# Optimization experiments

Hardware: AMD Instinct MI355X
Metric: run time of the kernel (lower is better)

## Reference

```python
import jax, jax.numpy as jnp
import numpy as np

HIDDEN = 1024
HEADS = 16
HEAD = HIDDEN // HEADS


def _ternary_weight(key, shape):
    g = jax.random.normal(key, shape, dtype=jnp.float32)
    return jnp.where(jnp.abs(g) < 0.6, 0.0, jnp.sign(g)).astype(jnp.float32)


def setup_inputs() -> dict:
    key = jax.random.key(0)
    ks = jax.random.split(key, 10)
    x = jax.random.normal(ks[0], (2, 2048, HIDDEN), dtype=jnp.float32)
    d = {"x": x}
    names = ["q", "k", "v", "o"]
    for i, n in enumerate(names):
        d[f"w_{n}"] = _ternary_weight(ks[1 + i], (HIDDEN, HIDDEN))
        d[f"s_{n}"] = jnp.float32(0.02)  # per-layer dequant scale
        d[f"b_{n}"] = jax.random.normal(ks[5 + i], (HIDDEN,), dtype=jnp.float32) * 0.02
    return d


def _tlin(x, w, s, b):
    # dequantized ternary linear: x @ (s * w).T + b
    return jnp.einsum("bsh,oh->bso", x, w) * s + b


def reference(x, w_q, s_q, b_q, w_k, s_k, b_k, w_v, s_v, b_v, w_o, s_o, b_o):
    B, S, H = x.shape
    def split_heads(t):
        return t.reshape(B, S, HEADS, HEAD).transpose(0, 2, 1, 3)  # [B, nH, S, hd]
    q = split_heads(_tlin(x, w_q, s_q, b_q))
    k = split_heads(_tlin(x, w_k, s_k, b_k))
    v = split_heads(_tlin(x, w_v, s_v, b_v))
    scores = jnp.einsum("bhqd,bhkd->bhqk", q, k) / jnp.sqrt(jnp.float32(HEAD))
    attn = jax.nn.softmax(scores, axis=-1)
    ctx = jnp.einsum("bhqk,bhkd->bhqd", attn, v)
    ctx = ctx.transpose(0, 2, 1, 3).reshape(B, S, H)
    return _tlin(ctx, w_o, s_o, b_o)
```

## Files before the change

kernel.cpp:

```cpp
#include <hip/hip_runtime.h>
#include <hip/hip_bf16.h>

typedef unsigned short u16;
typedef __bf16 bf16x8 __attribute__((ext_vector_type(8)));
typedef float f32x4 __attribute__((ext_vector_type(4)));
typedef unsigned short u16x8 __attribute__((ext_vector_type(8)));
typedef unsigned short u16x4 __attribute__((ext_vector_type(4)));

__device__ inline u16 f2bf(float f) {
    union { float f; unsigned u; } v; v.f = f;
    unsigned r = v.u + 0x7fffu + ((v.u >> 16) & 1u);
    return (u16)(r >> 16);
}

__device__ inline float bf2f(u16 b) {
    union { unsigned u; float f; } v; v.u = ((unsigned)b) << 16;
    return v.f;
}

__global__ void convert_kernel(const float* __restrict__ x,
                               const float* __restrict__ wq, const float* __restrict__ wk,
                               const float* __restrict__ wv, const float* __restrict__ wo,
                               u16* __restrict__ dst) {
    long g = (long)blockIdx.x * blockDim.x + threadIdx.x;
    const float* src; long base;
    const long GX = 1048576, GW = 262144;
    if (g < GX)            { src = x;  base = 0; }
    else if (g < GX + GW)  { src = wq; base = GX; }
    else if (g < GX + 2*GW){ src = wk; base = GX + GW; }
    else if (g < GX + 3*GW){ src = wv; base = GX + 2*GW; }
    else                   { src = wo; base = GX + 3*GW; }
    long rel = g - base;
    float4 v = reinterpret_cast<const float4*>(src)[rel];
    ushort4 o;
    o.x = f2bf(v.x); o.y = f2bf(v.y); o.z = f2bf(v.z); o.w = f2bf(v.w);
    reinterpret_cast<ushort4*>(dst)[g] = o;
}

#define LDP 72

__device__ inline void gemm_mainloop(const u16* __restrict__ A, const u16* __restrict__ W,
                                     int t0, int n0, u16* As, u16* Bs, f32x4 acc[4][4]) {
    const int tid = threadIdx.x;
    const int wid = tid >> 6, lane = tid & 63, quad = lane >> 4, ln = lane & 15;
    const int wm = wid >> 1, wn = wid & 1;
#pragma unroll
    for (int im = 0; im < 4; im++)
#pragma unroll
        for (int in = 0; in < 4; in++) acc[im][in] = (f32x4){0.f, 0.f, 0.f, 0.f};

    for (int k0 = 0; k0 < 1024; k0 += 64) {
#pragma unroll
        for (int i = 0; i < 4; i++) {
            int c = i * 256 + tid;
            int row = c >> 3, kc = c & 7;
            u16x8 av = *reinterpret_cast<const u16x8*>(A + (long)(t0 + row) * 1024 + k0 + kc * 8);
            u16x8 bv = *reinterpret_cast<const u16x8*>(W + (long)(n0 + row) * 1024 + k0 + kc * 8);
            *reinterpret_cast<u16x8*>(As + row * LDP + kc * 8) = av;
            *reinterpret_cast<u16x8*>(Bs + row * LDP + kc * 8) = bv;
        }
        __syncthreads();
#pragma unroll
        for (int ks = 0; ks < 2; ks++) {
            bf16x8 af[4], bf[4];
#pragma unroll
            for (int im = 0; im < 4; im++)
                af[im] = *reinterpret_cast<const bf16x8*>(As + (wm * 64 + im * 16 + ln) * LDP + ks * 32 + quad * 8);
#pragma unroll
            for (int in = 0; in < 4; in++)
                bf[in] = *reinterpret_cast<const bf16x8*>(Bs + (wn * 64 + in * 16 + ln) * LDP + ks * 32 + quad * 8);
#pragma unroll
            for (int im = 0; im < 4; im++)
#pragma unroll
                for (int in = 0; in < 4; in++)
                    acc[im][in] = __builtin_amdgcn_mfma_f32_16x16x32_bf16(af[im], bf[in], acc[im][in], 0, 0, 0);
        }
        __syncthreads();
    }
}

__global__ void qkv_gemm(const u16* __restrict__ x_bf,
                         const u16* __restrict__ wq, const u16* __restrict__ wk, const u16* __restrict__ wv,
                         const float* __restrict__ sq, const float* __restrict__ sk, const float* __restrict__ sv,
                         const float* __restrict__ bq, const float* __restrict__ bk, const float* __restrict__ bv,
                         u16* __restrict__ q_ws, u16* __restrict__ k_ws, u16* __restrict__ v_ws) {
    __shared__ u16 As[128 * LDP];
    __shared__ u16 Bs[128 * LDP];
    const int z = blockIdx.z;
    const u16* W   = (z == 0) ? wq : (z == 1) ? wk : wv;
    const float* sp = (z == 0) ? sq : (z == 1) ? sk : sv;
    const float* bp = (z == 0) ? bq : (z == 1) ? bk : bv;
    u16* dst = (z == 0) ? q_ws : (z == 1) ? k_ws : v_ws;
    const float extra = (z == 0) ? 0.125f : 1.0f;
    const int t0 = blockIdx.x * 128, n0 = blockIdx.y * 128;

    f32x4 acc[4][4];
    gemm_mainloop(x_bf, W, t0, n0, As, Bs, acc);

    const int tid = threadIdx.x;
    const int wid = tid >> 6, lane = tid & 63, quad = lane >> 4, ln = lane & 15;
    const int wm = wid >> 1, wn = wid & 1;
    const float s = sp[0] * extra;
#pragma unroll
    for (int in = 0; in < 4; in++) {
        int col = n0 + wn * 64 + in * 16 + ln;
        float bias = bp[col] * extra;
        int h = col >> 6, d = col & 63;
#pragma unroll
        for (int im = 0; im < 4; im++) {
            int rbase = t0 + wm * 64 + im * 16 + quad * 4;
#pragma unroll
            for (int j = 0; j < 4; j++) {
                int t = rbase + j;
                int b = t >> 11, ss = t & 2047;
                int bh = b * 16 + h;
                float val = acc[im][in][j] * s + bias;
                long idx = (z < 2) ? ((long)(bh * 2048 + ss) * 64 + d)
                                   : ((long)(bh * 64 + d) * 2048 + ss);
                dst[idx] = f2bf(val);
            }
        }
    }
}

__global__ void attn_kernel(const u16* __restrict__ q_ws, const u16* __restrict__ k_ws,
                            const u16* __restrict__ v_ws, u16* __restrict__ ctx) {
    __shared__ u16 Kt[64 * LDP];
    __shared__ u16 Vt[64 * LDP];
    __shared__ u16 Pt[128 * LDP];

    const int tid = threadIdx.x;
    const int wid = tid >> 6, lane = tid & 63, quad = lane >> 4, ln = lane & 15;
    const int bh = blockIdx.y;
    const int q0 = blockIdx.x * 128;
    const u16* qbase = q_ws + (long)bh * 2048 * 64;
    const u16* kbase = k_ws + (long)bh * 2048 * 64;
    const u16* vbase = v_ws + (long)bh * 64 * 2048;

    bf16x8 aq[2][2];
#pragma unroll
    for (int qt = 0; qt < 2; qt++)
#pragma unroll
        for (int ks = 0; ks < 2; ks++)
            aq[qt][ks] = *reinterpret_cast<const bf16x8*>(
                qbase + (long)(q0 + wid * 32 + qt * 16 + ln) * 64 + ks * 32 + quad * 8);

    f32x4 acc_o[2][4];
    float lsum[2] = {0.f, 0.f};
#pragma unroll
    for (int qt = 0; qt < 2; qt++)
#pragma unroll
        for (int dt = 0; dt < 4; dt++) acc_o[qt][dt] = (f32x4){0.f, 0.f, 0.f, 0.f};

    u16x8 kreg[2], vreg[2];
#pragma unroll
    for (int i = 0; i < 2; i++) {
        int c = i * 256 + tid;
        int row = c >> 3, kc = c & 7;
        kreg[i] = *reinterpret_cast<const u16x8*>(kbase + (long)row * 64 + kc * 8);
        vreg[i] = *reinterpret_cast<const u16x8*>(vbase + (long)row * 2048 + kc * 8);
    }

    for (int kt = 0; kt < 2048; kt += 64) {
#pragma unroll
        for (int i = 0; i < 2; i++) {
            int c = i * 256 + tid;
            int row = c >> 3, kc = c & 7;
            *reinterpret_cast<u16x8*>(Kt + row * LDP + kc * 8) = kreg[i];
            *reinterpret_cast<u16x8*>(Vt + row * LDP + kc * 8) = vreg[i];
        }
        if (kt + 64 < 2048) {
#pragma unroll
            for (int i = 0; i < 2; i++) {
                int c = i * 256 + tid;
                int row = c >> 3, kc = c & 7;
                kreg[i] = *reinterpret_cast<const u16x8*>(kbase + (long)(kt + 64 + row) * 64 + kc * 8);
                vreg[i] = *reinterpret_cast<const u16x8*>(vbase + (long)row * 2048 + (kt + 64) + kc * 8);
            }
        }
        __syncthreads();

#pragma unroll
        for (int k8 = 0; k8 < 4; k8++) {
            bf16x8 a0 = *reinterpret_cast<const bf16x8*>(Kt + (k8 * 16 + ln) * LDP + quad * 8);
            bf16x8 a1 = *reinterpret_cast<const bf16x8*>(Kt + (k8 * 16 + ln) * LDP + 32 + quad * 8);
#pragma unroll
            for (int qt = 0; qt < 2; qt++) {
                f32x4 t = (f32x4){0.f, 0.f, 0.f, 0.f};
                t = __builtin_amdgcn_mfma_f32_16x16x32_bf16(a0, aq[qt][0], t, 0, 0, 0);
                t = __builtin_amdgcn_mfma_f32_16x16x32_bf16(a1, aq[qt][1], t, 0, 0, 0);
                float p0 = __expf(t[0]), p1 = __expf(t[1]), p2 = __expf(t[2]), p3 = __expf(t[3]);
                u16x4 w;
                w.x = f2bf(p0); w.y = f2bf(p1); w.z = f2bf(p2); w.w = f2bf(p3);
                lsum[qt] += bf2f(w.x) + bf2f(w.y) + bf2f(w.z) + bf2f(w.w);
                *reinterpret_cast<u16x4*>(
                    Pt + (wid * 32 + qt * 16 + ln) * LDP + k8 * 16 + quad * 4) = w;
            }
        }

#pragma unroll
        for (int step = 0; step < 2; step++) {
            bf16x8 ap[2];
#pragma unroll
            for (int qt = 0; qt < 2; qt++)
                ap[qt] = *reinterpret_cast<const bf16x8*>(
                    Pt + (wid * 32 + qt * 16 + ln) * LDP + step * 32 + quad * 8);
#pragma unroll
            for (int dt = 0; dt < 4; dt++) {
                bf16x8 bv = *reinterpret_cast<const bf16x8*>(
                    Vt + (dt * 16 + ln) * LDP + step * 32 + quad * 8);
#pragma unroll
                for (int qt = 0; qt < 2; qt++)
                    acc_o[qt][dt] = __builtin_amdgcn_mfma_f32_16x16x32_bf16(ap[qt], bv, acc_o[qt][dt], 0, 0, 0);
            }
        }
        __syncthreads();
    }

    const int b = bh >> 4, h = bh & 15;
#pragma unroll
    for (int qt = 0; qt < 2; qt++) {
        float lt = lsum[qt];
        lt += __shfl_xor(lt, 16, 64);
        lt += __shfl_xor(lt, 32, 64);
#pragma unroll
        for (int j = 0; j < 4; j++) {
            float rinv = 1.0f / __shfl(lt, quad * 4 + j, 64);
            int t = b * 2048 + q0 + wid * 32 + qt * 16 + quad * 4 + j;
#pragma unroll
            for (int dt = 0; dt < 4; dt++) {
                float val = acc_o[qt][dt][j] * rinv;
                ctx[(long)t * 1024 + h * 64 + dt * 16 + ln] = f2bf(val);
            }
        }
    }
}

__global__ void o_gemm(const u16* __restrict__ ctx, const u16* __restrict__ wo,
                       const float* __restrict__ so, const float* __restrict__ bo,
                       float* __restrict__ out) {
    __shared__ u16 As[128 * LDP];
    __shared__ u16 Bs[128 * LDP];
    const int t0 = blockIdx.x * 128, n0 = blockIdx.y * 128;
    f32x4 acc[4][4];
    gemm_mainloop(ctx, wo, t0, n0, As, Bs, acc);

    const int tid = threadIdx.x;
    const int wid = tid >> 6, lane = tid & 63, quad = lane >> 4, ln = lane & 15;
    const int wm = wid >> 1, wn = wid & 1;
    const float s = so[0];
#pragma unroll
    for (int in = 0; in < 4; in++) {
        int col = n0 + wn * 64 + in * 16 + ln;
        float bias = bo[col];
#pragma unroll
        for (int im = 0; im < 4; im++) {
            int rbase = t0 + wm * 64 + im * 16 + quad * 4;
#pragma unroll
            for (int j = 0; j < 4; j++)
                out[(long)(rbase + j) * 1024 + col] = acc[im][in][j] * s + bias;
        }
    }
}

extern "C" void kernel_launch(void* const* d_in, const int* in_sizes, int n_in,
                              void* d_out, int out_size, void* d_ws, size_t ws_size,
                              hipStream_t stream) {
    const float* x   = (const float*)d_in[0];
    const float* w_q = (const float*)d_in[1];
    const float* s_q = (const float*)d_in[2];
    const float* b_q = (const float*)d_in[3];
    const float* w_k = (const float*)d_in[4];
    const float* s_k = (const float*)d_in[5];
    const float* b_k = (const float*)d_in[6];
    const float* w_v = (const float*)d_in[7];
    const float* s_v = (const float*)d_in[8];
    const float* b_v = (const float*)d_in[9];
    const float* w_o = (const float*)d_in[10];
    const float* s_o = (const float*)d_in[11];
    const float* b_o = (const float*)d_in[12];

    if (ws_size < (size_t)50331648) return;

    u16* ws     = (u16*)d_ws;
    u16* x_bf   = ws;
    u16* wq_bf  = x_bf  + 4194304;
    u16* wk_bf  = wq_bf + 1048576;
    u16* wv_bf  = wk_bf + 1048576;
    u16* wo_bf  = wv_bf + 1048576;
    u16* q_ws   = wo_bf + 1048576;
    u16* k_ws   = q_ws  + 4194304;
    u16* v_ws   = k_ws  + 4194304;
    u16* ctx_ws = v_ws  + 4194304;

    convert_kernel<<<dim3(8192), dim3(256), 0, stream>>>(x, w_q, w_k, w_v, w_o, ws);
    qkv_gemm<<<dim3(32, 8, 3), dim3(256), 0, stream>>>(x_bf, wq_bf, wk_bf, wv_bf,
                                                       s_q, s_k, s_v, b_q, b_k, b_v,
                                                       q_ws, k_ws, v_ws);
    attn_kernel<<<dim3(16, 32), dim3(256), 0, stream>>>(q_ws, k_ws, v_ws, ctx_ws);
    o_gemm<<<dim3(32, 8), dim3(256), 0, stream>>>(ctx_ws, wo_bf, s_o, b_o, (float*)d_out);
}
```

Measured before the change: 222.6 us.

## Use direct global-to-LDS loads with XOR swizzle, exp2 softmax, 512-thread attention

The GEMM mainloop now stages A and W tiles with global_load_lds straight into an unpadded, XOR-swizzled LDS layout instead of going through registers, and the fragment reads use the same swizzle to avoid bank conflicts. The Q scale folds in log2(e) so attention can use the hardware exp2 instruction in place of __expf. The attention kernel switches to 512 threads, with each wave handling 16 query rows instead of 32, which halves per-wave registers but doubles the waves sharing each K/V tile. These are several independent changes that trade code simplicity for less staging overhead and more parallelism.

Result: faster. 207.7 us (-6.7%).

```diff
diff --git a/kernel.cpp b/kernel.cpp
--- a/kernel.cpp
+++ b/kernel.cpp
@@ -3,19 +3,14 @@
 
 typedef unsigned short u16;
 typedef __bf16 bf16x8 __attribute__((ext_vector_type(8)));
+typedef __bf16 bf16x4 __attribute__((ext_vector_type(4)));
 typedef float f32x4 __attribute__((ext_vector_type(4)));
 typedef unsigned short u16x8 __attribute__((ext_vector_type(8)));
-typedef unsigned short u16x4 __attribute__((ext_vector_type(4)));
 
 __device__ inline u16 f2bf(float f) {
     union { float f; unsigned u; } v; v.f = f;
     unsigned r = v.u + 0x7fffu + ((v.u >> 16) & 1u);
     return (u16)(r >> 16);
-}
-
-__device__ inline float bf2f(u16 b) {
-    union { unsigned u; float f; } v; v.u = ((unsigned)b) << 16;
-    return v.f;
 }
 
 __global__ void convert_kernel(const float* __restrict__ x,
@@ -37,8 +32,6 @@
     reinterpret_cast<ushort4*>(dst)[g] = o;
 }
 
-#define LDP 72
-
 __device__ inline void gemm_mainloop(const u16* __restrict__ A, const u16* __restrict__ W,
                                      int t0, int n0, u16* As, u16* Bs, f32x4 acc[4][4]) {
     const int tid = threadIdx.x;
@@ -52,28 +45,40 @@
     for (int k0 = 0; k0 < 1024; k0 += 64) {
 #pragma unroll
         for (int i = 0; i < 4; i++) {
-            int c = i * 256 + tid;
-            int row = c >> 3, kc = c & 7;
-            u16x8 av = *reinterpret_cast<const u16x8*>(A + (long)(t0 + row) * 1024 + k0 + kc * 8);
-            u16x8 bv = *reinterpret_cast<const u16x8*>(W + (long)(n0 + row) * 1024 + k0 + kc * 8);
-            *reinterpret_cast<u16x8*>(As + row * LDP + kc * 8) = av;
-            *reinterpret_cast<u16x8*>(Bs + row * LDP + kc * 8) = bv;
+            int chunk = wid * 4 + i;
+            int b = chunk * 1024 + lane * 16;
+            int row = b >> 7;
+            int cb = (b & 127) ^ ((row & 7) << 4);
+            const u16* gA = A + (long)(t0 + row) * 1024 + k0 + (cb >> 1);
+            const u16* gB = W + (long)(n0 + row) * 1024 + k0 + (cb >> 1);
+            __builtin_amdgcn_global_load_lds((const __attribute__((address_space(1))) void*)gA,
+                                             (__attribute__((address_space(3))) void*)(As + chunk * 512),
+                                             16, 0, 0);
+            __builtin_amdgcn_global_load_lds((const __attribute__((address_space(1))) void*)gB,
+                                             (__attribute__((address_space(3))) void*)(Bs + chunk * 512),
+                                             16, 0, 0);
         }
         __syncthreads();
 #pragma unroll
         for (int ks = 0; ks < 2; ks++) {
-            bf16x8 af[4], bf[4];
+            bf16x8 af[4], bfr[4];
+#pragma unroll
+            for (int im = 0; im < 4; im++) {
+                int r = wm * 64 + im * 16 + ln;
+                int byt = (r * 128 + ks * 64 + quad * 16) ^ ((r & 7) << 4);
+                af[im] = *reinterpret_cast<const bf16x8*>((const char*)As + byt);
+            }
+#pragma unroll
+            for (int in = 0; in < 4; in++) {
+                int r = wn * 64 + in * 16 + ln;
+                int byt = (r * 128 + ks * 64 + quad * 16) ^ ((r & 7) << 4);
+                bfr[in] = *reinterpret_cast<const bf16x8*>((const char*)Bs + byt);
+            }
 #pragma unroll
             for (int im = 0; im < 4; im++)
-                af[im] = *reinterpret_cast<const bf16x8*>(As + (wm * 64 + im * 16 + ln) * LDP + ks * 32 + quad * 8);
-#pragma unroll
-            for (int in = 0; in < 4; in++)
-                bf[in] = *reinterpret_cast<const bf16x8*>(Bs + (wn * 64 + in * 16 + ln) * LDP + ks * 32 + quad * 8);
-#pragma unroll
-            for (int im = 0; im < 4; im++)
 #pragma unroll
                 for (int in = 0; in < 4; in++)
-                    acc[im][in] = __builtin_amdgcn_mfma_f32_16x16x32_bf16(af[im], bf[in], acc[im][in], 0, 0, 0);
+                    acc[im][in] = __builtin_amdgcn_mfma_f32_16x16x32_bf16(af[im], bfr[in], acc[im][in], 0, 0, 0);
         }
         __syncthreads();
     }
@@ -84,14 +89,14 @@
                          const float* __restrict__ sq, const float* __restrict__ sk, const float* __restrict__ sv,
                          const float* __restrict__ bq, const float* __restrict__ bk, const float* __restrict__ bv,
                          u16* __restrict__ q_ws, u16* __restrict__ k_ws, u16* __restrict__ v_ws) {
-    __shared__ u16 As[128 * LDP];
-    __shared__ u16 Bs[128 * LDP];
+    __shared__ __align__(16) u16 As[128 * 64];
+    __shared__ __align__(16) u16 Bs[128 * 64];
     const int z = blockIdx.z;
     const u16* W   = (z == 0) ? wq : (z == 1) ? wk : wv;
     const float* sp = (z == 0) ? sq : (z == 1) ? sk : sv;
     const float* bp = (z == 0) ? bq : (z == 1) ? bk : bv;
     u16* dst = (z == 0) ? q_ws : (z == 1) ? k_ws : v_ws;
-    const float extra = (z == 0) ? 0.125f : 1.0f;
+    const float extra = (z == 0) ? 0.125f * 1.44269504088896f : 1.0f;
     const int t0 = blockIdx.x * 128, n0 = blockIdx.y * 128;
 
     f32x4 acc[4][4];
@@ -123,8 +128,11 @@
     }
 }
 
-__global__ void attn_kernel(const u16* __restrict__ q_ws, const u16* __restrict__ k_ws,
-                            const u16* __restrict__ v_ws, u16* __restrict__ ctx) {
+#define LDP 72
+
+__global__ void __launch_bounds__(512)
+attn_kernel(const u16* __restrict__ q_ws, const u16* __restrict__ k_ws,
+            const u16* __restrict__ v_ws, u16* __restrict__ ctx) {
     __shared__ u16 Kt[64 * LDP];
     __shared__ u16 Vt[64 * LDP];
     __shared__ u16 Pt[128 * LDP];
@@ -137,46 +145,27 @@
     const u16* kbase = k_ws + (long)bh * 2048 * 64;
     const u16* vbase = v_ws + (long)bh * 64 * 2048;
 
-    bf16x8 aq[2][2];
-#pragma unroll
-    for (int qt = 0; qt < 2; qt++)
-#pragma unroll
-        for (int ks = 0; ks < 2; ks++)
-            aq[qt][ks] = *reinterpret_cast<const bf16x8*>(
-                qbase + (long)(q0 + wid * 32 + qt * 16 + ln) * 64 + ks * 32 + quad * 8);
-
-    f32x4 acc_o[2][4];
-    float lsum[2] = {0.f, 0.f};
-#pragma unroll
-    for (int qt = 0; qt < 2; qt++)
-#pragma unroll
-        for (int dt = 0; dt < 4; dt++) acc_o[qt][dt] = (f32x4){0.f, 0.f, 0.f, 0.f};
-
-    u16x8 kreg[2], vreg[2];
-#pragma unroll
-    for (int i = 0; i < 2; i++) {
-        int c = i * 256 + tid;
-        int row = c >> 3, kc = c & 7;
-        kreg[i] = *reinterpret_cast<const u16x8*>(kbase + (long)row * 64 + kc * 8);
-        vreg[i] = *reinterpret_cast<const u16x8*>(vbase + (long)row * 2048 + kc * 8);
-    }
+    bf16x8 aq[2];
+#pragma unroll
+    for (int ks = 0; ks < 2; ks++)
+        aq[ks] = *reinterpret_cast<const bf16x8*>(
+            qbase + (long)(q0 + wid * 16 + ln) * 64 + ks * 32 + quad * 8);
+
+    f32x4 acc_o[4];
+    float lsum = 0.f;
+#pragma unroll
+    for (int dt = 0; dt < 4; dt++) acc_o[dt] = (f32x4){0.f, 0.f, 0.f, 0.f};
+
+    const int srow = tid >> 3, skc = tid & 7;
+    u16x8 kreg = *reinterpret_cast<const u16x8*>(kbase + (long)srow * 64 + skc * 8);
+    u16x8 vreg = *reinterpret_cast<const u16x8*>(vbase + (long)srow * 2048 + skc * 8);
 
     for (int kt = 0; kt < 2048; kt += 64) {
-#pragma unroll
-        for (int i = 0; i < 2; i++) {
-            int c = i * 256 + tid;
-            int row = c >> 3, kc = c & 7;
-            *reinterpret_cast<u16x8*>(Kt + row * LDP + kc * 8) = kreg[i];
-            *reinterpret_cast<u16x8*>(Vt + row * LDP + kc * 8) = vreg[i];
-        }
+        *reinterpret_cast<u16x8*>(Kt + srow * LDP + skc * 8) = kreg;
+        *reinterpret_cast<u16x8*>(Vt + srow * LDP + skc * 8) = vreg;
         if (kt + 64 < 2048) {
-#pragma unroll
-            for (int i = 0; i < 2; i++) {
-                int c = i * 256 + tid;
-                int row = c >> 3, kc = c & 7;
-                kreg[i] = *reinterpret_cast<const u16x8*>(kbase + (long)(kt + 64 + row) * 64 + kc * 8);
-                vreg[i] = *reinterpret_cast<const u16x8*>(vbase + (long)row * 2048 + (kt + 64) + kc * 8);
-            }
+            kreg = *reinterpret_cast<const u16x8*>(kbase + (long)(kt + 64 + srow) * 64 + skc * 8);
+            vreg = *reinterpret_cast<const u16x8*>(vbase + (long)srow * 2048 + (kt + 64) + skc * 8);
         }
         __syncthreads();
 
@@ -184,54 +173,44 @@
         for (int k8 = 0; k8 < 4; k8++) {
             bf16x8 a0 = *reinterpret_cast<const bf16x8*>(Kt + (k8 * 16 + ln) * LDP + quad * 8);
             bf16x8 a1 = *reinterpret_cast<const bf16x8*>(Kt + (k8 * 16 + ln) * LDP + 32 + quad * 8);
-#pragma unroll
-            for (int qt = 0; qt < 2; qt++) {
-                f32x4 t = (f32x4){0.f, 0.f, 0.f, 0.f};
-                t = __builtin_amdgcn_mfma_f32_16x16x32_bf16(a0, aq[qt][0], t, 0, 0, 0);
-                t = __builtin_amdgcn_mfma_f32_16x16x32_bf16(a1, aq[qt][1], t, 0, 0, 0);
-                float p0 = __expf(t[0]), p1 = __expf(t[1]), p2 = __expf(t[2]), p3 = __expf(t[3]);
-                u16x4 w;
-                w.x = f2bf(p0); w.y = f2bf(p1); w.z = f2bf(p2); w.w = f2bf(p3);
-                lsum[qt] += bf2f(w.x) + bf2f(w.y) + bf2f(w.z) + bf2f(w.w);
-                *reinterpret_cast<u16x4*>(
-                    Pt + (wid * 32 + qt * 16 + ln) * LDP + k8 * 16 + quad * 4) = w;
-            }
+            f32x4 t = (f32x4){0.f, 0.f, 0.f, 0.f};
+            t = __builtin_amdgcn_mfma_f32_16x16x32_bf16(a0, aq[0], t, 0, 0, 0);
+            t = __builtin_amdgcn_mfma_f32_16x16x32_bf16(a1, aq[1], t, 0, 0, 0);
+            __bf16 p0 = (__bf16)__builtin_amdgcn_exp2f(t[0]);
+            __bf16 p1 = (__bf16)__builtin_amdgcn_exp2f(t[1]);
+            __bf16 p2 = (__bf16)__builtin_amdgcn_exp2f(t[2]);
+            __bf16 p3 = (__bf16)__builtin_amdgcn_exp2f(t[3]);
+            lsum += (float)p0 + (float)p1 + (float)p2 + (float)p3;
+            *reinterpret_cast<bf16x4*>(Pt + (wid * 16 + ln) * LDP + k8 * 16 + quad * 4)
+                = (bf16x4){p0, p1, p2, p3};
         }
 
 #pragma unroll
         for (int step = 0; step < 2; step++) {
-            bf16x8 ap[2];
-#pragma unroll
-            for (int qt = 0; qt < 2; qt++)
-                ap[qt] = *reinterpret_cast<const bf16x8*>(
-                    Pt + (wid * 32 + qt * 16 + ln) * LDP + step * 32 + quad * 8);
+            bf16x8 ap = *reinterpret_cast<const bf16x8*>(
+                Pt + (wid * 16 + ln) * LDP + step * 32 + quad * 8);
 #pragma unroll
             for (int dt = 0; dt < 4; dt++) {
                 bf16x8 bv = *reinterpret_cast<const bf16x8*>(
                     Vt + (dt * 16 + ln) * LDP + step * 32 + quad * 8);
-#pragma unroll
-                for (int qt = 0; qt < 2; qt++)
-                    acc_o[qt][dt] = __builtin_amdgcn_mfma_f32_16x16x32_bf16(ap[qt], bv, acc_o[qt][dt], 0, 0, 0);
+                acc_o[dt] = __builtin_amdgcn_mfma_f32_16x16x32_bf16(ap, bv, acc_o[dt], 0, 0, 0);
             }
         }
         __syncthreads();
     }
 
     const int b = bh >> 4, h = bh & 15;
-#pragma unroll
-    for (int qt = 0; qt < 2; qt++) {
-        float lt = lsum[qt];
-        lt += __shfl_xor(lt, 16, 64);
-        lt += __shfl_xor(lt, 32, 64);
-#pragma unroll
-        for (int j = 0; j < 4; j++) {
-            float rinv = 1.0f / __shfl(lt, quad * 4 + j, 64);
-            int t = b * 2048 + q0 + wid * 32 + qt * 16 + quad * 4 + j;
-#pragma unroll
-            for (int dt = 0; dt < 4; dt++) {
-                float val = acc_o[qt][dt][j] * rinv;
-                ctx[(long)t * 1024 + h * 64 + dt * 16 + ln] = f2bf(val);
-            }
+    float lt = lsum;
+    lt += __shfl_xor(lt, 16, 64);
+    lt += __shfl_xor(lt, 32, 64);
+#pragma unroll
+    for (int j = 0; j < 4; j++) {
+        float rinv = 1.0f / __shfl(lt, quad * 4 + j, 64);
+        int t = b * 2048 + q0 + wid * 16 + quad * 4 + j;
+#pragma unroll
+        for (int dt = 0; dt < 4; dt++) {
+            float val = acc_o[dt][j] * rinv;
+            ctx[(long)t * 1024 + h * 64 + dt * 16 + ln] = f2bf(val);
         }
     }
 }
@@ -239,8 +218,8 @@
 __global__ void o_gemm(const u16* __restrict__ ctx, const u16* __restrict__ wo,
                        const float* __restrict__ so, const float* __restrict__ bo,
                        float* __restrict__ out) {
-    __shared__ u16 As[128 * LDP];
-    __shared__ u16 Bs[128 * LDP];
+    __shared__ __align__(16) u16 As[128 * 64];
+    __shared__ __align__(16) u16 Bs[128 * 64];
     const int t0 = blockIdx.x * 128, n0 = blockIdx.y * 128;
     f32x4 acc[4][4];
     gemm_mainloop(ctx, wo, t0, n0, As, Bs, acc);
@@ -297,6 +276,6 @@
     qkv_gemm<<<dim3(32, 8, 3), dim3(256), 0, stream>>>(x_bf, wq_bf, wk_bf, wv_bf,
                                                        s_q, s_k, s_v, b_q, b_k, b_v,
                                                        q_ws, k_ws, v_ws);
-    attn_kernel<<<dim3(16, 32), dim3(256), 0, stream>>>(q_ws, k_ws, v_ws, ctx_ws);
+    attn_kernel<<<dim3(16, 32), dim3(512), 0, stream>>>(q_ws, k_ws, v_ws, ctx_ws);
     o_gemm<<<dim3(32, 8), dim3(256), 0, stream>>>(ctx_ws, wo_bf, s_o, b_o, (float*)d_out);
 }
```
